# Optimization experiments

Hardware: AMD Instinct MI355X
Metric: run time of the kernel (lower is better)

## Reference

```python
import jax, jax.numpy as jnp
import numpy as np

DIM = 1024
NUM_HEADS = 16
HEAD_DIM = DIM // NUM_HEADS
SCALE = HEAD_DIM ** -0.5


def setup_inputs() -> dict:
    key = jax.random.key(0)
    ks = jax.random.split(key, 5)
    B, N = 2, 2048
    x = jax.random.normal(ks[0], (B, N, DIM), dtype=jnp.float32)
    # nn.Linear weights: stored as [out, in]; we keep that convention.
    w_qkv = jax.random.normal(ks[1], (3 * DIM, DIM), dtype=jnp.float32) * (DIM ** -0.5)
    b_qkv = jax.random.normal(ks[2], (3 * DIM,), dtype=jnp.float32) * 0.02
    w_proj = jax.random.normal(ks[3], (DIM, DIM), dtype=jnp.float32) * (DIM ** -0.5)
    b_proj = jax.random.normal(ks[4], (DIM,), dtype=jnp.float32) * 0.02
    return {"x": x, "w_qkv": w_qkv, "b_qkv": b_qkv, "w_proj": w_proj, "b_proj": b_proj}


def reference(x, w_qkv, b_qkv, w_proj, b_proj):
    B, N, C = x.shape
    H, D = NUM_HEADS, HEAD_DIM
    qkv = x @ w_qkv.T + b_qkv                      # [B, N, 3C]
    qkv = qkv.reshape(B, N, 3, H, D)
    q = qkv[:, :, 0].transpose(0, 2, 1, 3)         # [B, H, N, D]
    k = qkv[:, :, 1].transpose(0, 2, 1, 3)
    v = qkv[:, :, 2].transpose(0, 2, 1, 3)
    attn = jnp.einsum("bhnd,bhmd->bhnm", q, k) * SCALE  # [B, H, N, N]
    attn = jax.nn.softmax(attn, axis=-1)
    out = jnp.einsum("bhnm,bhmd->bhnd", attn, v)   # [B, H, N, D]
    out = out.transpose(0, 2, 1, 3).reshape(B, N, C)
    return out @ w_proj.T + b_proj
```

## Files before the change

kernel.cpp:

```cpp
#include <hip/hip_runtime.h>
#include <math.h>

#define DIMC   1024
#define NHEADS 16
#define HDIM   64
#define BATCH  2
#define SEQ    2048

#define MTOT   (BATCH * SEQ)
#define QKVN   (3 * DIMC)
#define QKVSZ  ((size_t)BATCH * NHEADS * SEQ * HDIM)
#define HEADEL ((size_t)SEQ * HDIM)

#define QSCALE 0.18033688011112042f

typedef __attribute__((ext_vector_type(8))) short bf16x8;
typedef __attribute__((ext_vector_type(4))) short bf16x4;
typedef __attribute__((ext_vector_type(4))) float f32x4;

static __device__ inline short f2bf(float f) {
    union { float f; unsigned u; } v; v.f = f;
    unsigned r = v.u + 0x7fffu + ((v.u >> 16) & 1u);
    return (short)(r >> 16);
}

static __device__ inline unsigned cvt_pk_bf16(float lo, float hi) {
    unsigned r;
    asm("v_cvt_pk_bf16_f32 %0, %1, %2" : "=v"(r) : "v"(lo), "v"(hi));
    return r;
}

#if __has_builtin(__builtin_amdgcn_exp2f)
#define EXP2F(x) __builtin_amdgcn_exp2f(x)
#else
#define EXP2F(x) exp2f(x)
#endif

#define NXB  (MTOT * DIMC / 2048)
#define NWQB (QKVN * DIMC / 2048)
#define NWPB (DIMC * DIMC / 2048)

__global__ __launch_bounds__(256) void cast_all(
    const float* __restrict__ x,  const float* __restrict__ wq,
    const float* __restrict__ wp, short* __restrict__ xb,
    short* __restrict__ wqb, short* __restrict__ wpb)
{
    const float* in; short* out; int base;
    int bid = blockIdx.x;
    if (bid < NXB)              { in = x;  out = xb;  base = bid; }
    else if (bid < NXB + NWQB)  { in = wq; out = wqb; base = bid - NXB; }
    else                        { in = wp; out = wpb; base = bid - NXB - NWQB; }
    int i = (base * 256 + threadIdx.x) * 8;
    float4 a = *(const float4*)&in[i];
    float4 b = *(const float4*)&in[i + 4];
    bf16x8 o;
    o[0] = f2bf(a.x); o[1] = f2bf(a.y); o[2] = f2bf(a.z); o[3] = f2bf(a.w);
    o[4] = f2bf(b.x); o[5] = f2bf(b.y); o[6] = f2bf(b.z); o[7] = f2bf(b.w);
    *(bf16x8*)&out[i] = o;
}

__device__ __forceinline__ void gload16(const void* g, void* l) {
    __builtin_amdgcn_global_load_lds(
        (const __attribute__((address_space(1))) unsigned*)g,
        (__attribute__((address_space(3))) unsigned*)l, 16, 0, 0);
}

#define BAR() do { __builtin_amdgcn_s_barrier(); \
                   __builtin_amdgcn_sched_barrier(0); } while (0)
#define VWAIT8() asm volatile("s_waitcnt vmcnt(8)" ::: "memory")
#define VWAIT0() asm volatile("s_waitcnt vmcnt(0)" ::: "memory")

__device__ __forceinline__ void stage_panel128(const short* __restrict__ src,
                                               int row0, int k0,
                                               short* dst, int tid)
{
#pragma unroll
    for (int u = 0; u < 4; ++u) {
        const int gidx = u * 256 + tid;
        const int rl   = gidx >> 3;
        const int cc   = gidx & 7;
        gload16(&src[(size_t)(row0 + rl) * 1024 + k0 + ((cc ^ (rl & 7)) << 3)],
                &dst[(size_t)gidx << 3]);
    }
}

__device__ __forceinline__ void tile_compute(
    const short* Ac, const short* Bc, int wm, int wn,
    int lid, int quad, f32x4 (&acc)[4][4])
{
    bf16x8 bfr[4][2];
#pragma unroll
    for (int j2 = 0; j2 < 4; ++j2) {
        const int rb = wn + j2 * 16 + lid;
#pragma unroll
        for (int kk = 0; kk < 2; ++kk)
            bfr[j2][kk] = *(const bf16x8*)
                &Bc[rb * 64 + (((kk * 4 + quad) ^ (rb & 7)) << 3)];
    }
#pragma unroll
    for (int i2 = 0; i2 < 4; ++i2) {
        const int r = wm + i2 * 16 + lid;
        bf16x8 a0 = *(const bf16x8*)&Ac[r * 64 + (((quad) ^ (r & 7)) << 3)];
        bf16x8 a1 = *(const bf16x8*)&Ac[r * 64 + (((4 + quad) ^ (r & 7)) << 3)];
        __builtin_amdgcn_s_setprio(1);
#pragma unroll
        for (int j2 = 0; j2 < 4; ++j2) {
            acc[i2][j2] = __builtin_amdgcn_mfma_f32_16x16x32_bf16(
                a0, bfr[j2][0], acc[i2][j2], 0, 0, 0);
            acc[i2][j2] = __builtin_amdgcn_mfma_f32_16x16x32_bf16(
                a1, bfr[j2][1], acc[i2][j2], 0, 0, 0);
        }
        __builtin_amdgcn_s_setprio(0);
    }
}

__global__ __launch_bounds__(256, 2) void qkv_mfma(
    const short* __restrict__ xb,
    const short* __restrict__ wb,
    const float* __restrict__ bias,
    short* __restrict__ qkvb)
{
    __shared__ __attribute__((aligned(16))) short lds[2 * 16384];

    const int tid = threadIdx.x;
    const int T  = (blockIdx.x & 7) * 96 + (blockIdx.x >> 3);
    const int m0 = (T / 24) * 128;
    const int j0 = (T % 24) * 128;

    const int lane = tid & 63;
    const int w    = tid >> 6;
    const int quad = lane >> 4;
    const int lid  = lane & 15;
    const int wm = (w >> 1) * 64, wn = (w & 1) * 64;

    f32x4 acc[4][4];
#pragma unroll
    for (int i = 0; i < 4; ++i)
#pragma unroll
        for (int j = 0; j < 4; ++j) acc[i][j] = (f32x4){0.f, 0.f, 0.f, 0.f};

    stage_panel128(xb, m0, 0, lds,        tid);
    stage_panel128(wb, j0, 0, lds + 8192, tid);

#pragma unroll 2
    for (int kt = 0; kt < 15; ++kt) {
        const int cb = (kt & 1) << 14;
        const int nb = (~kt & 1) << 14;
        const int k1 = (kt + 1) << 6;
        const short* Ac = lds + cb;
        const short* Bc = Ac + 8192;

        stage_panel128(xb, m0, k1, lds + nb,        tid);
        stage_panel128(wb, j0, k1, lds + nb + 8192, tid);

        VWAIT8(); BAR();
        tile_compute(Ac, Bc, wm, wn, lid, quad, acc);
        BAR();
    }
    {
        const short* Ac = lds + 16384;
        VWAIT0(); BAR();
        tile_compute(Ac, Ac + 8192, wm, wn, lid, quad, acc);
    }

    const int s = j0 >> 10;

    if (s == 0) {
#pragma unroll
        for (int jb = 0; jb < 4; ++jb) {
            const int jj = j0 + wn + jb * 16 + lid;
            const int hh = (jj & 1023) >> 6;
            const int dd = jj & 63;
            const float bv = bias[jj];
#pragma unroll
            for (int i = 0; i < 4; ++i)
#pragma unroll
                for (int r = 0; r < 4; ++r) {
                    const int mrow = m0 + wm + i * 16 + quad * 4 + r;
                    const int b_ = mrow >> 11, nn = mrow & 2047;
                    qkvb[((size_t)(b_ * NHEADS + hh) * SEQ + nn) * HDIM + dd] =
                        f2bf((acc[i][jb][r] + bv) * QSCALE);
                }
        }
    } else if (s == 1) {
#pragma unroll
        for (int jb = 0; jb < 4; ++jb) {
            const int jj = j0 + wn + jb * 16 + lid;
            const int hh = (jj & 1023) >> 6;
            const int dd = jj & 63;
            const int c2 = dd >> 5;
            const int qd = (dd >> 3) & 3;
            const int jo = dd & 7;
            const float bv = bias[jj];
#pragma unroll
            for (int i = 0; i < 4; ++i) {
                const int mrow0 = m0 + wm + i * 16;
                const int b_ = mrow0 >> 11;
                const int n0 = mrow0 & 2047;
                const int t32 = n0 >> 5;
                const int i16 = (n0 >> 4) & 1;
                const int c = quad & 1;
                const int lidb = (i16 * 2 + (quad >> 1)) * 4;
                size_t base = QKVSZ + (size_t)(b_ * NHEADS + hh) * HEADEL +
                              (size_t)(t32 * 4 + c2 * 2 + c) * 512 +
                              (qd * 16 + lidb) * 8 + jo;
#pragma unroll
                for (int r = 0; r < 4; ++r)
                    qkvb[base + r * 8] = f2bf(acc[i][jb][r] + bv);
            }
        }
    } else {
#pragma unroll
        for (int jb = 0; jb < 4; ++jb) {
            const int jj = j0 + wn + jb * 16 + lid;
            const int hh = (jj & 1023) >> 6;
            const int dd = jj & 63;
            const int fb = dd >> 4;
            const int dl = dd & 15;
            const float bv = bias[jj];
#pragma unroll
            for (int i = 0; i < 4; ++i) {
                const int mrow0 = m0 + wm + i * 16 + quad * 4;
                const int b_ = mrow0 >> 11, n0 = mrow0 & 2047;
                const int t32 = n0 >> 5;
                const int i16 = (n0 >> 4) & 1;
                const int quadpp = i16 * 2 + (quad >> 1);
                bf16x4 o;
#pragma unroll
                for (int r = 0; r < 4; ++r) o[r] = f2bf(acc[i][jb][r] + bv);
                *(bf16x4*)&qkvb[2 * QKVSZ + (size_t)(b_ * NHEADS + hh) * HEADEL +
                                (size_t)(t32 * 4 + fb) * 512 +
                                (quadpp * 16 + dl) * 8 + (quad & 1) * 4] = o;
            }
        }
    }
}

__device__ __forceinline__ void load_kv(
    const short* __restrict__ Kf, const short* __restrict__ Vf,
    int t, int lane, bf16x8 (&aK)[2][2], bf16x8 (&aV)[4])
{
#pragma unroll
    for (int c = 0; c < 2; ++c)
#pragma unroll
        for (int c2 = 0; c2 < 2; ++c2)
            aK[c][c2] = *(const bf16x8*)&Kf[(size_t)(t * 4 + c2 * 2 + c) * 512 +
                                            lane * 8];
#pragma unroll
    for (int fb = 0; fb < 4; ++fb)
        aV[fb] = *(const bf16x8*)&Vf[(size_t)(t * 4 + fb) * 512 + lane * 8];
}

__device__ __forceinline__ void attn_chunk(
    const bf16x8 (&aK)[2][2], const bf16x8 (&aV)[4],
    const bf16x8 (&bQ)[4][2], const bf16x8& ones8,
    f32x4 (&O)[4][4], f32x4 (&L)[4])
{
#pragma unroll
    for (int g = 0; g < 4; ++g) {
        f32x4 s0 = (f32x4){0.f, 0.f, 0.f, 0.f};
        f32x4 s1 = (f32x4){0.f, 0.f, 0.f, 0.f};
        __builtin_amdgcn_s_setprio(1);
        s0 = __builtin_amdgcn_mfma_f32_16x16x32_bf16(aK[0][0], bQ[g][0], s0, 0, 0, 0);
        s1 = __builtin_amdgcn_mfma_f32_16x16x32_bf16(aK[1][0], bQ[g][0], s1, 0, 0, 0);
        s0 = __builtin_amdgcn_mfma_f32_16x16x32_bf16(aK[0][1], bQ[g][1], s0, 0, 0, 0);
        s1 = __builtin_amdgcn_mfma_f32_16x16x32_bf16(aK[1][1], bQ[g][1], s1, 0, 0, 0);
        __builtin_amdgcn_s_setprio(0);
        union { unsigned u[4]; bf16x8 v; } P;
        P.u[0] = cvt_pk_bf16(EXP2F(s0[0]), EXP2F(s0[1]));
        P.u[1] = cvt_pk_bf16(EXP2F(s0[2]), EXP2F(s0[3]));
        P.u[2] = cvt_pk_bf16(EXP2F(s1[0]), EXP2F(s1[1]));
        P.u[3] = cvt_pk_bf16(EXP2F(s1[2]), EXP2F(s1[3]));
        __builtin_amdgcn_s_setprio(1);
        L[g] = __builtin_amdgcn_mfma_f32_16x16x32_bf16(ones8, P.v, L[g], 0, 0, 0);
#pragma unroll
        for (int fb = 0; fb < 4; ++fb)
            O[g][fb] = __builtin_amdgcn_mfma_f32_16x16x32_bf16(
                aV[fb], P.v, O[g][fb], 0, 0, 0);
        __builtin_amdgcn_s_setprio(0);
    }
}

__global__ __launch_bounds__(256, 2) void attn_mfma(
    const short* __restrict__ qkvb,
    short* __restrict__ aob)
{
    __shared__ float Osm[4][4][4][64];
    __shared__ float Lsm[3][64];

    const int tid  = threadIdx.x;
    const int sp   = tid >> 6;
    const int lane = tid & 63;
    const int quad = lane >> 4;
    const int lid  = lane & 15;

    const int bid  = blockIdx.x;
    const int xcd  = bid & 7;
    const int slot = bid >> 3;
    const int pair = xcd * 4 + (slot >> 5);
    const int qblk = slot & 31;
    const int h = pair & 15;
    const int b = pair >> 4;
    const int qbase = qblk * 64;

    const short* Qh = qkvb + (size_t)(b * NHEADS + h) * HEADEL;
    const short* Kf = Qh + QKVSZ;
    const short* Vf = qkvb + 2 * QKVSZ + (size_t)(b * NHEADS + h) * HEADEL;

    bf16x8 bQ[4][2];
#pragma unroll
    for (int g = 0; g < 4; ++g)
#pragma unroll
        for (int c = 0; c < 2; ++c)
            bQ[g][c] = *(const bf16x8*)&Qh[(size_t)(qbase + g * 16 + lid) * HDIM +
                                           c * 32 + quad * 8];

    f32x4 O[4][4];
    f32x4 L[4];
#pragma unroll
    for (int g = 0; g < 4; ++g) {
        L[g] = (f32x4){0.f, 0.f, 0.f, 0.f};
#pragma unroll
        for (int fb = 0; fb < 4; ++fb) O[g][fb] = (f32x4){0.f, 0.f, 0.f, 0.f};
    }
    const bf16x8 ones8 = {(short)0x3F80, (short)0x3F80, (short)0x3F80, (short)0x3F80,
                          (short)0x3F80, (short)0x3F80, (short)0x3F80, (short)0x3F80};

    bf16x8 aK0[2][2], aV0[4], aK1[2][2], aV1[4];
    const int t0 = sp * (SEQ / 128);
    load_kv(Kf, Vf, t0, lane, aK0, aV0);
#pragma unroll 2
    for (int cc = 0; cc < 16; cc += 2) {
        load_kv(Kf, Vf, t0 + cc + 1, lane, aK1, aV1);
        attn_chunk(aK0, aV0, bQ, ones8, O, L);
        if (cc + 2 < 16)
            load_kv(Kf, Vf, t0 + cc + 2, lane, aK0, aV0);
        attn_chunk(aK1, aV1, bQ, ones8, O, L);
    }

    if (sp != 0 && quad == 0)
#pragma unroll
        for (int g = 0; g < 4; ++g) Lsm[sp - 1][g * 16 + lid] = L[g][0];

    if (sp == 1) {
#pragma unroll
        for (int g = 0; g < 4; ++g)
#pragma unroll
            for (int fb = 0; fb < 4; ++fb)
#pragma unroll
                for (int r = 0; r < 4; ++r)
                    Osm[g][fb][r][lane] = O[g][fb][r];
    }
    __syncthreads();
    if (sp == 0) {
#pragma unroll
        for (int g = 0; g < 4; ++g)
#pragma unroll
            for (int fb = 0; fb < 4; ++fb)
#pragma unroll
                for (int r = 0; r < 4; ++r)
                    O[g][fb][r] += Osm[g][fb][r][lane];
    }
    __syncthreads();
    if (sp == 3) {
#pragma unroll
        for (int g = 0; g < 4; ++g)
#pragma unroll
            for (int fb = 0; fb < 4; ++fb)
#pragma unroll
                for (int r = 0; r < 4; ++r)
                    Osm[g][fb][r][lane] = O[g][fb][r];
    }
    __syncthreads();
    if (sp == 2) {
#pragma unroll
        for (int g = 0; g < 4; ++g)
#pragma unroll
            for (int fb = 0; fb < 4; ++fb)
#pragma unroll
                for (int r = 0; r < 4; ++r)
                    O[g][fb][r] += Osm[g][fb][r][lane];
    }
    __syncthreads();
    if (sp == 2) {
#pragma unroll
        for (int g = 0; g < 4; ++g)
#pragma unroll
            for (int fb = 0; fb < 4; ++fb)
#pragma unroll
                for (int r = 0; r < 4; ++r)
                    Osm[g][fb][r][lane] = O[g][fb][r];
    }
    __syncthreads();
    if (sp == 0) {
#pragma unroll
        for (int g = 0; g < 4; ++g) {
            const float lt = L[g][0] + Lsm[0][g * 16 + lid] +
                             Lsm[1][g * 16 + lid] + Lsm[2][g * 16 + lid];
            const float inv = 1.f / lt;
            const int n = qbase + g * 16 + lid;
            size_t base = ((size_t)(b * SEQ + n)) * DIMC + h * HDIM;
#pragma unroll
            for (int fb = 0; fb < 4; ++fb) {
                bf16x4 o;
#pragma unroll
                for (int r = 0; r < 4; ++r)
                    o[r] = f2bf((O[g][fb][r] + Osm[g][fb][r][lane]) * inv);
                *(bf16x4*)&aob[base + fb * 16 + quad * 4] = o;
            }
        }
    }
}

__global__ __launch_bounds__(256, 2) void proj_mfma(
    const short* __restrict__ ab,
    const short* __restrict__ wb,
    const float* __restrict__ bias,
    float* __restrict__ out)
{
    __shared__ __attribute__((aligned(16))) short Asm[2 * 64 * 32];
    __shared__ __attribute__((aligned(16))) short Bsm[2 * 128 * 32];

    const int tid = threadIdx.x;
    const int m0 = blockIdx.y * 64;
    const int j0 = blockIdx.x * 128;

    const int lane = tid & 63;
    const int w    = tid >> 6;
    const int quad = lane >> 4;
    const int lid  = lane & 15;
    const int wm = (w >> 1) * 32, wn = (w & 1) * 64;

    const int srow = lane >> 2;
    const int skc  = (lane & 3) * 8;

    f32x4 acc[2][4];
#pragma unroll
    for (int i = 0; i < 2; ++i)
#pragma unroll
        for (int j = 0; j < 4; ++j) acc[i][j] = (f32x4){0.f, 0.f, 0.f, 0.f};

    for (int k0 = 0; k0 < 1024; k0 += 64) {
        __syncthreads();
#pragma unroll
        for (int u = 0; u < 2; ++u) {
            const int combo = w * 2 + u;
            const int hh = combo >> 2, rb = combo & 3;
            const int row = rb * 16 + srow;
            gload16(&ab[(size_t)(m0 + row) * 1024 + k0 + hh * 32 + skc],
                    &Asm[hh * 2048 + row * 32 + skc]);
        }
#pragma unroll
        for (int u = 0; u < 4; ++u) {
            const int combo = w * 4 + u;
            const int hh = combo >> 3, rb = combo & 7;
            const int row = rb * 16 + srow;
            gload16(&wb[(size_t)(j0 + row) * 1024 + k0 + hh * 32 + skc],
                    &Bsm[hh * 4096 + row * 32 + skc]);
        }
        __syncthreads();

#pragma unroll
        for (int hh = 0; hh < 2; ++hh) {
            bf16x8 af[2], bfr[4];
#pragma unroll
            for (int i = 0; i < 2; ++i)
                af[i] = *(const bf16x8*)&Asm[hh * 2048 + (wm + i * 16 + lid) * 32 + quad * 8];
#pragma unroll
            for (int j = 0; j < 4; ++j)
                bfr[j] = *(const bf16x8*)&Bsm[hh * 4096 + (wn + j * 16 + lid) * 32 + quad * 8];
#pragma unroll
            for (int i = 0; i < 2; ++i)
#pragma unroll
                for (int j = 0; j < 4; ++j)
                    acc[i][j] = __builtin_amdgcn_mfma_f32_16x16x32_bf16(
                        af[i], bfr[j], acc[i][j], 0, 0, 0);
        }
    }

#pragma unroll
    for (int jb = 0; jb < 4; ++jb) {
        const int jj = j0 + wn + jb * 16 + lid;
        const float bv = bias[jj];
#pragma unroll
        for (int i = 0; i < 2; ++i)
#pragma unroll
            for (int r = 0; r < 4; ++r) {
                const int mrow = m0 + wm + i * 16 + quad * 4 + r;
                out[(size_t)mrow * DIMC + jj] = acc[i][jb][r] + bv;
            }
    }
}

extern "C" void kernel_launch(void* const* d_in, const int* in_sizes, int n_in,
                              void* d_out, int out_size, void* d_ws, size_t ws_size,
                              hipStream_t stream) {
    const float* x      = (const float*)d_in[0];
    const float* w_qkv  = (const float*)d_in[1];
    const float* b_qkv  = (const float*)d_in[2];
    const float* w_proj = (const float*)d_in[3];
    const float* b_proj = (const float*)d_in[4];
    float* out = (float*)d_out;

    short* qkvb   = (short*)d_ws;
    short* xb     = qkvb + 3 * QKVSZ;
    short* wqkvb  = xb + (size_t)MTOT * DIMC;
    short* wprojb = wqkvb + (size_t)QKVN * DIMC;
    short* aob    = wprojb + (size_t)DIMC * DIMC;

    cast_all<<<NXB + NWQB + NWPB, 256, 0, stream>>>(x, w_qkv, w_proj,
                                                    xb, wqkvb, wprojb);

    qkv_mfma<<<768, 256, 0, stream>>>(xb, wqkvb, b_qkv, qkvb);

    attn_mfma<<<BATCH * NHEADS * (SEQ / 64), 256, 0, stream>>>(qkvb, aob);

    dim3 g3(DIMC / 128, MTOT / 64);
    proj_mfma<<<g3, 256, 0, stream>>>(aob, wprojb, b_proj, out);
}
```

Measured before the change: 167.5 us.

## Double-buffer projection GEMM with async LDS prefetch and swizzled layout

Rewrites the output-projection kernel's K loop to double-buffer LDS. It prefetches the next 64-wide K panel with global_load_lds while computing the current one, using a partial vmcnt wait instead of two full syncthreads per iteration. It also switches the staging to the XOR-swizzled 64-column layout used by the QKV GEMM, to reduce LDS bank conflicts. This doubles LDS use per block, which may limit occupancy. The projection is only one of several kernels, so the overall effect is bounded.

```diff
diff --git a/kernel.cpp b/kernel.cpp
--- a/kernel.cpp
+++ b/kernel.cpp
@@ -68,6 +68,7 @@
 #define BAR() do { __builtin_amdgcn_s_barrier(); \
                    __builtin_amdgcn_sched_barrier(0); } while (0)
 #define VWAIT8() asm volatile("s_waitcnt vmcnt(8)" ::: "memory")
+#define VWAIT6() asm volatile("s_waitcnt vmcnt(6)" ::: "memory")
 #define VWAIT0() asm volatile("s_waitcnt vmcnt(0)" ::: "memory")
 
 __device__ __forceinline__ void stage_panel128(const short* __restrict__ src,
@@ -84,6 +85,21 @@
     }
 }
 
+template<int U>
+__device__ __forceinline__ void stage_panelU(const short* __restrict__ src,
+                                             int row0, int k0,
+                                             short* dst, int tid)
+{
+#pragma unroll
+    for (int u = 0; u < U; ++u) {
+        const int gidx = u * 256 + tid;
+        const int rl   = gidx >> 3;
+        const int cc   = gidx & 7;
+        gload16(&src[(size_t)(row0 + rl) * 1024 + k0 + ((cc ^ (rl & 7)) << 3)],
+                &dst[(size_t)gidx << 3]);
+    }
+}
+
 __device__ __forceinline__ void tile_compute(
     const short* Ac, const short* Bc, int wm, int wn,
     int lid, int quad, f32x4 (&acc)[4][4])
@@ -99,6 +115,36 @@
     }
 #pragma unroll
     for (int i2 = 0; i2 < 4; ++i2) {
+        const int r = wm + i2 * 16 + lid;
+        bf16x8 a0 = *(const bf16x8*)&Ac[r * 64 + (((quad) ^ (r & 7)) << 3)];
+        bf16x8 a1 = *(const bf16x8*)&Ac[r * 64 + (((4 + quad) ^ (r & 7)) << 3)];
+        __builtin_amdgcn_s_setprio(1);
+#pragma unroll
+        for (int j2 = 0; j2 < 4; ++j2) {
+            acc[i2][j2] = __builtin_amdgcn_mfma_f32_16x16x32_bf16(
+                a0, bfr[j2][0], acc[i2][j2], 0, 0, 0);
+            acc[i2][j2] = __builtin_amdgcn_mfma_f32_16x16x32_bf16(
+                a1, bfr[j2][1], acc[i2][j2], 0, 0, 0);
+        }
+        __builtin_amdgcn_s_setprio(0);
+    }
+}
+
+__device__ __forceinline__ void tile_computeP(
+    const short* Ac, const short* Bc, int wm, int wn,
+    int lid, int quad, f32x4 (&acc)[2][4])
+{
+    bf16x8 bfr[4][2];
+#pragma unroll
+    for (int j2 = 0; j2 < 4; ++j2) {
+        const int rb = wn + j2 * 16 + lid;
+#pragma unroll
+        for (int kk = 0; kk < 2; ++kk)
+            bfr[j2][kk] = *(const bf16x8*)
+                &Bc[rb * 64 + (((kk * 4 + quad) ^ (rb & 7)) << 3)];
+    }
+#pragma unroll
+    for (int i2 = 0; i2 < 2; ++i2) {
         const int r = wm + i2 * 16 + lid;
         bf16x8 a0 = *(const bf16x8*)&Ac[r * 64 + (((quad) ^ (r & 7)) << 3)];
         bf16x8 a1 = *(const bf16x8*)&Ac[r * 64 + (((4 + quad) ^ (r & 7)) << 3)];
@@ -418,8 +464,7 @@
     const float* __restrict__ bias,
     float* __restrict__ out)
 {
-    __shared__ __attribute__((aligned(16))) short Asm[2 * 64 * 32];
-    __shared__ __attribute__((aligned(16))) short Bsm[2 * 128 * 32];
+    __shared__ __attribute__((aligned(16))) short lds[2 * 12288];
 
     const int tid = threadIdx.x;
     const int m0 = blockIdx.y * 64;
@@ -431,51 +476,34 @@
     const int lid  = lane & 15;
     const int wm = (w >> 1) * 32, wn = (w & 1) * 64;
 
-    const int srow = lane >> 2;
-    const int skc  = (lane & 3) * 8;
-
     f32x4 acc[2][4];
 #pragma unroll
     for (int i = 0; i < 2; ++i)
 #pragma unroll
         for (int j = 0; j < 4; ++j) acc[i][j] = (f32x4){0.f, 0.f, 0.f, 0.f};
 
-    for (int k0 = 0; k0 < 1024; k0 += 64) {
-        __syncthreads();
-#pragma unroll
-        for (int u = 0; u < 2; ++u) {
-            const int combo = w * 2 + u;
-            const int hh = combo >> 2, rb = combo & 3;
-            const int row = rb * 16 + srow;
-            gload16(&ab[(size_t)(m0 + row) * 1024 + k0 + hh * 32 + skc],
-                    &Asm[hh * 2048 + row * 32 + skc]);
-        }
-#pragma unroll
-        for (int u = 0; u < 4; ++u) {
-            const int combo = w * 4 + u;
-            const int hh = combo >> 3, rb = combo & 7;
-            const int row = rb * 16 + srow;
-            gload16(&wb[(size_t)(j0 + row) * 1024 + k0 + hh * 32 + skc],
-                    &Bsm[hh * 4096 + row * 32 + skc]);
-        }
-        __syncthreads();
-
-#pragma unroll
-        for (int hh = 0; hh < 2; ++hh) {
-            bf16x8 af[2], bfr[4];
-#pragma unroll
-            for (int i = 0; i < 2; ++i)
-                af[i] = *(const bf16x8*)&Asm[hh * 2048 + (wm + i * 16 + lid) * 32 + quad * 8];
-#pragma unroll
-            for (int j = 0; j < 4; ++j)
-                bfr[j] = *(const bf16x8*)&Bsm[hh * 4096 + (wn + j * 16 + lid) * 32 + quad * 8];
-#pragma unroll
-            for (int i = 0; i < 2; ++i)
-#pragma unroll
-                for (int j = 0; j < 4; ++j)
-                    acc[i][j] = __builtin_amdgcn_mfma_f32_16x16x32_bf16(
-                        af[i], bfr[j], acc[i][j], 0, 0, 0);
-        }
+    stage_panelU<2>(ab, m0, 0, lds,        tid);
+    stage_panelU<4>(wb, j0, 0, lds + 4096, tid);
+
+#pragma unroll 2
+    for (int kt = 0; kt < 15; ++kt) {
+        const int cb = (kt & 1) * 12288;
+        const int nb = (~kt & 1) * 12288;
+        const int k1 = (kt + 1) << 6;
+        const short* Ac = lds + cb;
+        const short* Bc = Ac + 4096;
+
+        stage_panelU<2>(ab, m0, k1, lds + nb,        tid);
+        stage_panelU<4>(wb, j0, k1, lds + nb + 4096, tid);
+
+        VWAIT6(); BAR();
+        tile_computeP(Ac, Bc, wm, wn, lid, quad, acc);
+        BAR();
+    }
+    {
+        const short* Ac = lds + 12288;
+        VWAIT0(); BAR();
+        tile_computeP(Ac, Ac + 4096, wm, wn, lid, quad, acc);
     }
 
 #pragma unroll
```

After: 167.9 us. No clear change (+0.2%).
